# Performance work log

Hardware: AMD Instinct MI355X
Metric: run time of the kernel (lower is better)

Reference implementation:

```python
import jax, jax.numpy as jnp
import numpy as np

NUM_EMBED = 1024
EMBED_DIM = 256
COMMIT_COEF = 0.25


def setup_inputs() -> dict:
    key = jax.random.key(0)
    k1, k2 = jax.random.split(key)
    input = jax.random.normal(k1, (16, EMBED_DIM, 64, 64), dtype=jnp.float32)
    codebook = jax.random.normal(k2, (NUM_EMBED, EMBED_DIM), dtype=jnp.float32)
    last_used = jnp.zeros((NUM_EMBED,), dtype=jnp.int32)
    return {"input": input, "codebook": codebook, "last_used": last_used}


def reference(input, codebook, last_used):
    # (B, D, H, W) -> (B, H, W, D) -> (N, D)
    x = jnp.moveaxis(input, 1, -1)
    batch_shape = x.shape[:-1]
    flat = x.reshape(-1, x.shape[-1])  # (N, D)

    # Squared euclidean distances; argmin is identical to argmin of torch.cdist
    # (monotone sqrt), computed as a GEMM for efficiency.
    d2 = (
        jnp.sum(flat * flat, axis=-1, keepdims=True)
        - 2.0 * (flat @ codebook.T)
        + jnp.sum(codebook * codebook, axis=-1)
    )  # (N, K)
    idxes = jnp.argmin(d2, axis=-1).reshape(batch_shape)  # (B, H, W)

    embed = codebook[idxes]                 # (B, H, W, D) gather
    embed = jnp.moveaxis(embed, -1, 1)      # (B, D, H, W)

    # replace_unused bookkeeping (scatter). With last_used starting at zero,
    # last_used >= replace_after never triggers, so no codebook rewrite occurs.
    is_used = jnp.zeros((NUM_EMBED,), dtype=bool).at[idxes.ravel()].set(True)
    new_last_used = jnp.where(is_used, jnp.int32(0), last_used + jnp.int32(1))

    sg = jax.lax.stop_gradient
    codebook_loss = jnp.mean((sg(embed) - input) ** 2)
    commitment_loss = jnp.mean((embed - sg(input)) ** 2)
    vq_loss = codebook_loss + COMMIT_COEF * commitment_loss

    return idxes, embed, vq_loss, new_last_used
```

## Files before the change

### kernel.cpp

```cpp
#include <hip/hip_runtime.h>

#define NUM_EMBED 1024
#define EMBED_DIM 256
#define SPATIAL 4096
#define NROWS 65536
#define EMBED_ELEMS 16777216
#define HMARGIN 0.05f

typedef _Float16 half8 __attribute__((ext_vector_type(8)));
typedef float f32x4 __attribute__((ext_vector_type(4)));

__device__ __forceinline__ unsigned fkey(float f) {
  unsigned u = __float_as_uint(f);
  return (u & 0x80000000u) ? ~u : (u | 0x80000000u);
}

#define UPD(V1, V2, I1, S, I)                            \
  { float _s = (S);                                      \
    if (_s < (V1)) { (V2) = (V1); (V1) = _s; (I1) = (I); } \
    else if (_s < (V2)) { (V2) = _s; } }

#define MERGE(V1A, V2A, I1A, V1B, V2B, I1B)                       \
  { if ((V1B) < (V1A)) { (V2A) = fminf((V1A), (V2B)); (V1A) = (V1B); (I1A) = (I1B); } \
    else { (V2A) = fminf((V2A), (V1B)); } }

__global__ __launch_bounds__(256) void k_init(const float* __restrict__ cb,
                                              int* __restrict__ used,
                                              int* __restrict__ flagcount,
                                              float* __restrict__ cnorm,
                                              _Float16* __restrict__ cb16) {
  int bid = blockIdx.x, tid = threadIdx.x;
  if (bid == 0) {
    used[tid] = 0; used[tid + 256] = 0; used[tid + 512] = 0; used[tid + 768] = 0;
    if (tid == 0) *flagcount = 0;
  } else if (bid <= 64) {
    int c = (bid - 1) * 16 + (tid >> 4);
    int l = tid & 15;
    const float4* p = (const float4*)(cb + c * EMBED_DIM + l * 16);
    float s = 0.f;
#pragma unroll
    for (int j = 0; j < 4; ++j) {
      float4 v = p[j];
      s += v.x * v.x + v.y * v.y + v.z * v.z + v.w * v.w;
    }
#pragma unroll
    for (int off = 1; off < 16; off <<= 1) s += __shfl_xor(s, off, 16);
    if (l == 0) cnorm[c] = s;
  } else {
    int gid = (bid - 65) * 256 + tid;
    int ch = gid >> 9;
    int rem = gid & 511;
    int ks = rem >> 6;
    int lg = (rem >> 4) & 3;
    int ln = rem & 15;
    int S = (ch * 16 + ln) * 256 + ks * 32 + lg * 8;
    const float4* src = (const float4*)(cb + S);
    float4 a = src[0], b = src[1];
    half8 h;
    h[0] = (_Float16)a.x; h[1] = (_Float16)a.y; h[2] = (_Float16)a.z; h[3] = (_Float16)a.w;
    h[4] = (_Float16)b.x; h[5] = (_Float16)b.y; h[6] = (_Float16)b.z; h[7] = (_Float16)b.w;
    *(half8*)(cb16 + gid * 8) = h;
  }
}

__global__ __launch_bounds__(256, 2) void k_score(const float* __restrict__ in,
                                                  const _Float16* __restrict__ cb16,
                                                  const float* __restrict__ cnorm,
                                                  float* __restrict__ out_idx,
                                                  int* __restrict__ idxi,
                                                  int* __restrict__ flagged,
                                                  int* __restrict__ flagcount,
                                                  int* __restrict__ used) {
  __shared__ _Float16 As[4][4096];
  __shared__ float cn_lds[1024];
  int tid = threadIdx.x;
  int lane = tid & 63;
  int wave = tid >> 6;
  int ln = lane & 15;
  int lg = lane >> 4;
  int r0 = blockIdx.x << 6;
  const float* Ain = in + ((r0 >> 12) * (EMBED_DIM * SPATIAL)) + (r0 & 4095);

  {
    char* scratch = (char*)As[0];
    int row = tid & 63;
    int kq = tid >> 6;
    const float* p0 = Ain + row;
#pragma unroll
    for (int j = 0; j < 8; ++j) {
      int kc = kq * 8 + j;
      half8 hv;
#pragma unroll
      for (int q = 0; q < 8; ++q) hv[q] = (_Float16)p0[(kc * 8 + q) * SPATIAL];
      *(half8*)(scratch + kc * 1024 + row * 16) = hv;
    }
#pragma unroll
    for (int i = 0; i < 4; ++i) cn_lds[tid + 256 * i] = 0.5f * cnorm[tid + 256 * i];
  }
  __syncthreads();
  half8 xf[8][4];
  {
    const char* scratch = (const char*)As[0];
#pragma unroll
    for (int ks = 0; ks < 8; ++ks)
#pragma unroll
      for (int nf = 0; nf < 4; ++nf)
        xf[ks][nf] = *(const half8*)(scratch + (ks * 4 + lg) * 1024 + (nf * 16 + ln) * 16);
  }
  __syncthreads();

  char* buf = (char*)As[0] + wave * 8192;
  const _Float16* src0 = cb16 + wave * 65536 + lane * 8;

  half8 stg[8];
#pragma unroll
  for (int i = 0; i < 8; ++i) stg[i] = *(const half8*)(src0 + i * 512);
#pragma unroll
  for (int i = 0; i < 8; ++i) *(half8*)(buf + i * 1024 + lane * 16) = stg[i];

  float sv1[4] = {3e38f, 3e38f, 3e38f, 3e38f};
  float sv2[4] = {3e38f, 3e38f, 3e38f, 3e38f};
  int si1[4] = {0, 0, 0, 0};
  int afo = lg * 256 + ln * 16;

#pragma unroll 1
  for (int c = 0; c < 16; ++c) {
    if (c < 15) {
      const _Float16* ps = src0 + (c + 1) * 4096;
#pragma unroll
      for (int i = 0; i < 8; ++i) stg[i] = *(const half8*)(ps + i * 512);
    }
    f32x4 acc[4] = {};
    __builtin_amdgcn_s_setprio(1);
#pragma unroll
    for (int ks = 0; ks < 8; ++ks) {
      half8 af = *(const half8*)(buf + ks * 1024 + afo);
#pragma unroll
      for (int nf = 0; nf < 4; ++nf)
        acc[nf] = __builtin_amdgcn_mfma_f32_16x16x32_f16(af, xf[ks][nf], acc[nf], 0, 0, 0);
    }
    __builtin_amdgcn_s_setprio(0);
    int cb0 = wave * 256 + c * 16;
    float cna[4];
    *(float4*)cna = *(const float4*)(cn_lds + cb0 + lg * 4);
    int ib0 = cb0 + lg * 4;
#pragma unroll
    for (int nf = 0; nf < 4; ++nf) {
      float v1a = cna[0] - acc[nf][0], v2a = 3e38f;
      int i1a = ib0;
#pragma unroll
      for (int r = 1; r < 4; ++r) UPD(v1a, v2a, i1a, cna[r] - acc[nf][r], ib0 + r);
      MERGE(sv1[nf], sv2[nf], si1[nf], v1a, v2a, i1a);
    }
    if (c < 15) {
#pragma unroll
      for (int i = 0; i < 8; ++i) *(half8*)(buf + i * 1024 + lane * 16) = stg[i];
    }
  }

#pragma unroll
  for (int nf = 0; nf < 4; ++nf) {
#pragma unroll
    for (int off = 16; off < 64; off <<= 1) {
      float ov1 = __shfl_xor(sv1[nf], off);
      float ov2 = __shfl_xor(sv2[nf], off);
      int oi = __shfl_xor(si1[nf], off);
      if (ov1 < sv1[nf]) { sv2[nf] = fminf(sv1[nf], ov2); sv1[nf] = ov1; si1[nf] = oi; }
      else { sv2[nf] = fminf(sv2[nf], ov1); }
    }
  }

  __syncthreads();
  float* mv1 = (float*)As[0];
  float* mv2 = mv1 + 256;
  int* mi1 = (int*)(mv2 + 256);
  if (lg == 0) {
#pragma unroll
    for (int nf = 0; nf < 4; ++nf) {
      int slot = wave * 64 + nf * 16 + ln;
      mv1[slot] = sv1[nf]; mv2[slot] = sv2[nf]; mi1[slot] = si1[nf];
    }
  }
  __syncthreads();
  if (tid < 64) {
    float v1 = mv1[tid], v2 = mv2[tid];
    int i1 = mi1[tid];
#pragma unroll
    for (int w = 1; w < 4; ++w)
      MERGE(v1, v2, i1, mv1[w * 64 + tid], mv2[w * 64 + tid], mi1[w * 64 + tid]);
    int grow = r0 + tid;
    out_idx[grow] = (float)i1;
    idxi[grow] = i1;
    if (v2 - v1 < HMARGIN) {
      int p = atomicAdd(flagcount, 1);
      flagged[p] = grow;
    } else {
      used[i1] = 1;
    }
  }
}

__global__ __launch_bounds__(256) void k_cleanup(const float* __restrict__ in,
                                                 const float* __restrict__ cb,
                                                 const float* __restrict__ cnorm,
                                                 const int* __restrict__ flagged,
                                                 const int* __restrict__ flagcount,
                                                 float* __restrict__ out_idx,
                                                 int* __restrict__ idxi,
                                                 int* __restrict__ used) {
  __shared__ float xs[256];
  __shared__ unsigned long long red[4];
  int tid = threadIdx.x;
  int lane = tid & 63;
  int wave = tid >> 6;
  int sub = lane & 15;
  int cg = lane >> 4;
  int nf = *flagcount;
  const float4* cb4 = (const float4*)cb;
  for (int fi = blockIdx.x; fi < nf; fi += 2048) {
    int row = flagged[fi];
    int b = row >> 12, s = row & 4095;
    xs[tid] = in[b * (EMBED_DIM * SPATIAL) + tid * SPATIAL + s];
    __syncthreads();
    const float4* xs4 = (const float4*)xs;
    float4 x0 = xs4[sub], x1 = xs4[16 + sub], x2 = xs4[32 + sub], x3 = xs4[48 + sub];
    unsigned long long best = ~0ull;
    int c0 = wave * 256 + cg;
#pragma unroll 4
    for (int g = 0; g < 64; ++g) {
      int c = c0 + g * 4;
      const float4* crow = cb4 + c * 64 + sub;
      float4 d0 = crow[0], d1 = crow[16], d2 = crow[32], d3 = crow[48];
      float p = d0.x * x0.x + d0.y * x0.y + d0.z * x0.z + d0.w * x0.w;
      p += d1.x * x1.x + d1.y * x1.y + d1.z * x1.z + d1.w * x1.w;
      p += d2.x * x2.x + d2.y * x2.y + d2.z * x2.z + d2.w * x2.w;
      p += d3.x * x3.x + d3.y * x3.y + d3.z * x3.z + d3.w * x3.w;
#pragma unroll
      for (int off = 1; off < 16; off <<= 1) p += __shfl_xor(p, off);
      if (sub == 0) {
        float sc = cnorm[c] - 2.0f * p;
        unsigned long long k = ((unsigned long long)fkey(sc) << 32) | (unsigned)c;
        best = k < best ? k : best;
      }
    }
    {
      unsigned long long o = __shfl_xor(best, 16); best = o < best ? o : best;
      o = __shfl_xor(best, 32); best = o < best ? o : best;
    }
    if (lane == 0) red[wave] = best;
    __syncthreads();
    if (tid == 0) {
      unsigned long long bb = red[0];
#pragma unroll
      for (int w = 1; w < 4; ++w) { unsigned long long o = red[w]; bb = o < bb ? o : bb; }
      int idx = (int)(bb & 0xffffffffull);
      out_idx[row] = (float)idx;
      idxi[row] = idx;
      used[idx] = 1;
    }
    __syncthreads();
  }
}

__global__ __launch_bounds__(256) void k_gather(const float* __restrict__ in,
                                                const float* __restrict__ cb,
                                                const int* __restrict__ idxi,
                                                float* __restrict__ embed_out,
                                                double* __restrict__ partials) {
  __shared__ float E[32][257];
  __shared__ int idx_l[32];
  __shared__ float wsum[4];
  int tid = threadIdx.x;
  int lane = tid & 63;
  int wave = tid >> 6;
  int r0 = blockIdx.x << 5;
  int b = r0 >> 12;
  int s0 = r0 & 4095;
  if (tid < 32) idx_l[tid] = idxi[r0 + tid];
  __syncthreads();
  const float4* cb4 = (const float4*)cb;
#pragma unroll
  for (int jj = 0; jj < 8; ++jj) {
    int j = wave * 8 + jj;
    float4 v = cb4[idx_l[j] * 64 + lane];
    E[j][lane * 4 + 0] = v.x;
    E[j][lane * 4 + 1] = v.y;
    E[j][lane * 4 + 2] = v.z;
    E[j][lane * 4 + 3] = v.w;
  }
  __syncthreads();
  float lsum = 0.f;
  int s = lane & 31;
  int dpar = lane >> 5;
  const float* inp = in + b * (EMBED_DIM * SPATIAL) + s0 + s;
  float* outp = embed_out + b * (EMBED_DIM * SPATIAL) + s0 + s;
#pragma unroll 8
  for (int i = 0; i < 32; ++i) {
    int d = wave * 64 + i * 2 + dpar;
    float e = E[s][d];
    float x = inp[d * SPATIAL];
    outp[d * SPATIAL] = e;
    float df = e - x;
    lsum += df * df;
  }
#pragma unroll
  for (int off = 1; off < 64; off <<= 1) lsum += __shfl_xor(lsum, off, 64);
  if (lane == 0) wsum[wave] = lsum;
  __syncthreads();
  if (tid == 0)
    partials[blockIdx.x] = (double)(wsum[0] + wsum[1] + wsum[2] + wsum[3]);
}

__global__ __launch_bounds__(256) void k_tail(const double* __restrict__ partials,
                                              const int* __restrict__ used,
                                              const int* __restrict__ last_used,
                                              float* __restrict__ out_loss,
                                              float* __restrict__ out_lu) {
  int tid = threadIdx.x;
  double s = 0.0;
  for (int i = tid; i < 2048; i += 256) s += partials[i];
#pragma unroll
  for (int off = 1; off < 64; off <<= 1) s += __shfl_xor(s, off, 64);
  __shared__ double sd[4];
  if ((tid & 63) == 0) sd[tid >> 6] = s;
  __syncthreads();
  if (tid == 0) {
    double total = sd[0] + sd[1] + sd[2] + sd[3];
    out_loss[0] = (float)(1.25 * total / (double)EMBED_ELEMS);
  }
  for (int i = tid; i < NUM_EMBED; i += 256)
    out_lu[i] = used[i] ? 0.0f : (float)(last_used[i] + 1);
}

extern "C" void kernel_launch(void* const* d_in, const int* in_sizes, int n_in,
                              void* d_out, int out_size, void* d_ws, size_t ws_size,
                              hipStream_t stream) {
  const float* in = (const float*)d_in[0];
  const float* cb = (const float*)d_in[1];
  const int* last_used = (const int*)d_in[2];

  float* out = (float*)d_out;
  float* out_idx = out;
  float* embed_out = out + NROWS;
  float* out_loss = embed_out + EMBED_ELEMS;
  float* out_lu = out_loss + 1;

  _Float16* cb16 = (_Float16*)d_ws;
  double* partials = (double*)(cb16 + NUM_EMBED * EMBED_DIM);
  int* flagged = (int*)(partials + 4096);
  int* flagcount = flagged + NROWS;
  int* idxi = flagcount + 16;
  int* used = idxi + NROWS;
  float* cnorm = (float*)(used + NUM_EMBED);

  hipLaunchKernelGGL(k_init, dim3(193), dim3(256), 0, stream, cb, used, flagcount, cnorm, cb16);
  hipLaunchKernelGGL(k_score, dim3(1024), dim3(256), 0, stream, in, cb16, cnorm, out_idx,
                     idxi, flagged, flagcount, used);
  hipLaunchKernelGGL(k_cleanup, dim3(2048), dim3(256), 0, stream, in, cb, cnorm, flagged,
                     flagcount, out_idx, idxi, used);
  hipLaunchKernelGGL(k_gather, dim3(2048), dim3(256), 0, stream, in, cb, idxi, embed_out,
                     partials);
  hipLaunchKernelGGL(k_tail, dim3(1), dim3(256), 0, stream, partials, used, last_used,
                     out_loss, out_lu);
}
```

Measured before the change: 133.4 us.

## Derive VQ loss from score-kernel distances to drop input re-read in gather

```diff
diff --git a/kernel.cpp b/kernel.cpp
--- a/kernel.cpp
+++ b/kernel.cpp
@@ -70,9 +70,11 @@
                                                   int* __restrict__ idxi,
                                                   int* __restrict__ flagged,
                                                   int* __restrict__ flagcount,
-                                                  int* __restrict__ used) {
+                                                  int* __restrict__ used,
+                                                  double* __restrict__ partials) {
   __shared__ _Float16 As[4][4096];
   __shared__ float cn_lds[1024];
+  __shared__ float sred[4];
   int tid = threadIdx.x;
   int lane = tid & 63;
   int wave = tid >> 6;
@@ -81,6 +83,7 @@
   int r0 = blockIdx.x << 6;
   const float* Ain = in + ((r0 >> 12) * (EMBED_DIM * SPATIAL)) + (r0 & 4095);
 
+  float sx = 0.f;
   {
     char* scratch = (char*)As[0];
     int row = tid & 63;
@@ -91,7 +94,11 @@
       int kc = kq * 8 + j;
       half8 hv;
 #pragma unroll
-      for (int q = 0; q < 8; ++q) hv[q] = (_Float16)p0[(kc * 8 + q) * SPATIAL];
+      for (int q = 0; q < 8; ++q) {
+        float xv = p0[(kc * 8 + q) * SPATIAL];
+        sx += xv * xv;
+        hv[q] = (_Float16)xv;
+      }
       *(half8*)(scratch + kc * 1024 + row * 16) = hv;
     }
 #pragma unroll
@@ -157,6 +164,10 @@
       for (int i = 0; i < 8; ++i) *(half8*)(buf + i * 1024 + lane * 16) = stg[i];
     }
   }
+
+#pragma unroll
+  for (int off = 1; off < 64; off <<= 1) sx += __shfl_xor(sx, off, 64);
+  if (lane == 0) sred[wave] = sx;
 
 #pragma unroll
   for (int nf = 0; nf < 4; ++nf) {
@@ -197,6 +208,12 @@
     } else {
       used[i1] = 1;
     }
+    float hsum = v1;
+#pragma unroll
+    for (int off = 1; off < 64; off <<= 1) hsum += __shfl_xor(hsum, off, 64);
+    if (tid == 0)
+      partials[blockIdx.x] =
+          (double)(sred[0] + sred[1] + sred[2] + sred[3]) + 2.0 * (double)hsum;
   }
 }
 
@@ -262,14 +279,11 @@
   }
 }
 
-__global__ __launch_bounds__(256) void k_gather(const float* __restrict__ in,
-                                                const float* __restrict__ cb,
+__global__ __launch_bounds__(256) void k_gather(const float* __restrict__ cb,
                                                 const int* __restrict__ idxi,
-                                                float* __restrict__ embed_out,
-                                                double* __restrict__ partials) {
+                                                float* __restrict__ embed_out) {
   __shared__ float E[32][257];
   __shared__ int idx_l[32];
-  __shared__ float wsum[4];
   int tid = threadIdx.x;
   int lane = tid & 63;
   int wave = tid >> 6;
@@ -289,26 +303,14 @@
     E[j][lane * 4 + 3] = v.w;
   }
   __syncthreads();
-  float lsum = 0.f;
   int s = lane & 31;
   int dpar = lane >> 5;
-  const float* inp = in + b * (EMBED_DIM * SPATIAL) + s0 + s;
   float* outp = embed_out + b * (EMBED_DIM * SPATIAL) + s0 + s;
 #pragma unroll 8
   for (int i = 0; i < 32; ++i) {
     int d = wave * 64 + i * 2 + dpar;
-    float e = E[s][d];
-    float x = inp[d * SPATIAL];
-    outp[d * SPATIAL] = e;
-    float df = e - x;
-    lsum += df * df;
-  }
-#pragma unroll
-  for (int off = 1; off < 64; off <<= 1) lsum += __shfl_xor(lsum, off, 64);
-  if (lane == 0) wsum[wave] = lsum;
-  __syncthreads();
-  if (tid == 0)
-    partials[blockIdx.x] = (double)(wsum[0] + wsum[1] + wsum[2] + wsum[3]);
+    outp[d * SPATIAL] = E[s][d];
+  }
 }
 
 __global__ __launch_bounds__(256) void k_tail(const double* __restrict__ partials,
@@ -318,7 +320,7 @@
                                               float* __restrict__ out_lu) {
   int tid = threadIdx.x;
   double s = 0.0;
-  for (int i = tid; i < 2048; i += 256) s += partials[i];
+  for (int i = tid; i < 1024; i += 256) s += partials[i];
 #pragma unroll
   for (int off = 1; off < 64; off <<= 1) s += __shfl_xor(s, off, 64);
   __shared__ double sd[4];
@@ -355,11 +357,10 @@
 
   hipLaunchKernelGGL(k_init, dim3(193), dim3(256), 0, stream, cb, used, flagcount, cnorm, cb16);
   hipLaunchKernelGGL(k_score, dim3(1024), dim3(256), 0, stream, in, cb16, cnorm, out_idx,
-                     idxi, flagged, flagcount, used);
+                     idxi, flagged, flagcount, used, partials);
   hipLaunchKernelGGL(k_cleanup, dim3(2048), dim3(256), 0, stream, in, cb, cnorm, flagged,
                      flagcount, out_idx, idxi, used);
-  hipLaunchKernelGGL(k_gather, dim3(2048), dim3(256), 0, stream, in, cb, idxi, embed_out,
-                     partials);
+  hipLaunchKernelGGL(k_gather, dim3(2048), dim3(256), 0, stream, cb, idxi, embed_out);
   hipLaunchKernelGGL(k_tail, dim3(1), dim3(256), 0, stream, partials, used, last_used,
                      out_loss, out_lu);
 }
```

Result: slower. 139.2 us (+4.4%).
